# Performance work log

Hardware: AMD Instinct MI355X
Metric: run time of the kernel (lower is better)

Reference implementation:

```python
import jax, jax.numpy as jnp
import numpy as np

N_NODES = 100000
N_EDGES = 1200000
D_IN = 64
D_OUT = 64


def setup_inputs() -> dict:
    key = jax.random.key(0)
    ks = jax.random.split(key, 8)
    feat = jax.random.normal(ks[0], (N_NODES, D_IN), dtype=jnp.float32)
    src = jax.random.randint(ks[1], (N_EDGES,), 0, N_NODES, dtype=jnp.int32)
    dst = jax.random.randint(ks[2], (N_EDGES,), 0, N_NODES, dtype=jnp.int32)
    edge_weight = jax.random.uniform(ks[3], (N_EDGES, 1), dtype=jnp.float32)
    edge_mask = jax.random.uniform(ks[4], (N_EDGES, 1), dtype=jnp.float32)
    W_self = jax.random.normal(ks[5], (D_OUT, D_IN), dtype=jnp.float32) * (1.0 / np.sqrt(D_IN))
    b_self = jnp.zeros((D_OUT,), dtype=jnp.float32)
    W_neigh = jax.random.normal(ks[6], (D_OUT, D_IN), dtype=jnp.float32) * (1.0 / np.sqrt(D_IN))
    b_neigh = jnp.zeros((D_OUT,), dtype=jnp.float32)
    return {"feat": feat, "src": src, "dst": dst, "edge_weight": edge_weight,
            "edge_mask": edge_mask, "W_self": W_self, "b_self": b_self,
            "W_neigh": W_neigh, "b_neigh": b_neigh}


def reference(feat, src, dst, edge_weight, edge_mask, W_self, b_self, W_neigh, b_neigh):
    # message: gather src feats, scale by per-edge weight and mask  -> [E, D_IN]
    msg = feat[src] * edge_weight * edge_mask
    # mean scatter-reduce over incoming edges per dst node
    neigh_sum = jax.ops.segment_sum(msg, dst, num_segments=N_NODES)  # [N, D_IN]
    deg = jax.ops.segment_sum(jnp.ones((msg.shape[0],), dtype=feat.dtype), dst,
                              num_segments=N_NODES)  # [N]
    h_neigh = neigh_sum / jnp.maximum(deg, 1.0)[:, None]  # zero-degree nodes -> 0 (DGL mean semantics)
    # dual linear fuse
    rst = (feat @ W_self.T + b_self) + (h_neigh @ W_neigh.T + b_neigh)
    return rst
```

## Files before the change

### kernel.cpp

```cpp
#include <hip/hip_runtime.h>

#define NB_MAX   1568
#define CAP      1024
#define BT_EDGES 4096
#define BT_TPB   512
#define EPE      8

typedef __attribute__((ext_vector_type(4))) float floatx4;
typedef __attribute__((ext_vector_type(8))) short bf16x8;

__device__ __forceinline__ unsigned short f32_to_bf16(float f) {
  unsigned u = __float_as_uint(f);
  u = (u + 0x7fffu + ((u >> 16) & 1u)) >> 16;
  return (unsigned short)u;
}
__device__ __forceinline__ float bf16lo(unsigned u) {
  return __uint_as_float(u << 16);
}
__device__ __forceinline__ float bf16hi(unsigned u) {
  return __uint_as_float(u & 0xffff0000u);
}
__device__ __forceinline__ unsigned pack2(float a, float b) {
  return (unsigned)f32_to_bf16(a) | ((unsigned)f32_to_bf16(b) << 16);
}
__device__ __forceinline__ bf16x8 zero_bf16x8() {
  bf16x8 v;
#pragma unroll
  for (int i = 0; i < 8; ++i) v[i] = 0;
  return v;
}

__global__ __launch_bounds__(BT_TPB) void k_build(
    const float* __restrict__ feat, const int* __restrict__ src,
    const int* __restrict__ dst, const float* __restrict__ ew,
    const float* __restrict__ em, const float* __restrict__ Ws,
    const float* __restrict__ Wn, int* __restrict__ gCursor,
    uint2* __restrict__ recs, unsigned short* __restrict__ featb,
    unsigned short* __restrict__ Wb, int E, int nChunks, int nB) {
  __shared__ unsigned stageA[BT_EDGES];
  __shared__ unsigned short stageW[BT_EDGES];
  __shared__ int A[NB_MAX];
  __shared__ int B[NB_MAX];
  __shared__ int waveSums[8];

  const int t = threadIdx.x;
  const int lane = t & 63;
  const int wvid = t >> 6;
  const int e0 = blockIdx.x * BT_EDGES;
  const int eEnd = min(e0 + BT_EDGES, E);
  const int nLocal = eEnd - e0;

  for (int i = t; i < NB_MAX; i += BT_TPB) B[i] = 0;
  __syncthreads();

  int dreg[EPE];
#pragma unroll
  for (int k = 0; k < EPE; ++k) {
    int i = e0 + k * BT_TPB + t;
    dreg[k] = -1;
    if (i < eEnd) {
      int d = dst[i];
      dreg[k] = d;
      atomicAdd(&B[d >> 6], 1);
    }
  }
  __syncthreads();

  {
    const int EPT = 4;
    int b0 = t * EPT;
    int v[EPT];
    int sum = 0;
#pragma unroll
    for (int j = 0; j < EPT; ++j) {
      v[j] = (b0 + j < nB) ? B[b0 + j] : 0;
      sum += v[j];
    }
    int x = sum;
#pragma unroll
    for (int d = 1; d < 64; d <<= 1) {
      int y = __shfl_up(x, d, 64);
      if (lane >= d) x += y;
    }
    if (lane == 63) waveSums[wvid] = x;
    __syncthreads();
    int wprefix = 0;
    for (int i = 0; i < wvid; ++i) wprefix += waveSums[i];
    int run = wprefix + x - sum;
#pragma unroll
    for (int j = 0; j < EPT; ++j) {
      if (b0 + j < nB) A[b0 + j] = run;
      run += v[j];
    }
  }
  __syncthreads();

  for (int i = t; i < nB; i += BT_TPB) {
    int c = B[i];
    int l = A[i];
    int g = c ? atomicAdd(&gCursor[i], c) : 0;
    A[i] = i * CAP + g - l;
    B[i] = l;
  }
  __syncthreads();

#pragma unroll
  for (int k = 0; k < EPE; ++k) {
    int i = e0 + k * BT_TPB + t;
    if (i < eEnd) {
      int d = dreg[k];
      int r = atomicAdd(&B[d >> 6], 1);
      stageA[r] = (unsigned)src[i] | ((unsigned)(d & 63) << 17);
      float w = ew[i] * em[i];
      int wf = (int)(w * 65535.0f + 0.5f);
      stageW[r] = (unsigned short)min(wf, 65535);
    }
  }
  __syncthreads();

  for (int i = t; i < nLocal; i += BT_TPB) {
    int lo = 0, hi = nB;
    while (lo < hi) {
      int mid = (lo + hi) >> 1;
      if (B[mid] > i) hi = mid; else lo = mid + 1;
    }
    int pos = A[lo] + i;
    if (pos < (lo + 1) * CAP)
      recs[pos] = make_uint2(stageA[i], (unsigned)stageW[i]);
  }

  for (int c = blockIdx.x * BT_TPB + t; c < nChunks; c += gridDim.x * BT_TPB) {
    const float4* fp = reinterpret_cast<const float4*>(feat) + (size_t)c * 2;
    float4 a = fp[0], b = fp[1];
    uint4 o;
    o.x = pack2(a.x, a.y);
    o.y = pack2(a.z, a.w);
    o.z = pack2(b.x, b.y);
    o.w = pack2(b.z, b.w);
    reinterpret_cast<uint4*>(featb)[c] = o;
  }

  if (blockIdx.x == 0) {
    for (int i = t; i < 1024; i += BT_TPB) {
      int j = i >> 4, c4 = i & 15;
      float4 w4 = reinterpret_cast<const float4*>(Ws)[i];
      float4 n4 = reinterpret_cast<const float4*>(Wn)[i];
      *reinterpret_cast<uint2*>(&Wb[j * 128 + c4 * 4]) =
          make_uint2(pack2(w4.x, w4.y), pack2(w4.z, w4.w));
      *reinterpret_cast<uint2*>(&Wb[j * 128 + 64 + c4 * 4]) =
          make_uint2(pack2(n4.x, n4.y), pack2(n4.z, n4.w));
    }
  }
}

__global__ __launch_bounds__(256, 6) void sage_gather_gemm(
    const unsigned short* __restrict__ featb,
    const unsigned short* __restrict__ Wb, const int* __restrict__ gCursor,
    const uint2* __restrict__ recs, const float* __restrict__ bs,
    const float* __restrict__ bn, float* __restrict__ out, int N) {
  __shared__ unsigned short An[64][72];
  __shared__ uint2 recsL[CAP];
  __shared__ int cntS[64], offS[64], curS[64];

  const int t = threadIdx.x;
  const int b = blockIdx.x;
  const int n0 = b * 64;
  const int base = b * CAP;
  const int cb = min(gCursor[b], CAP);

  if (t < 64) cntS[t] = 0;
  __syncthreads();

  for (int i = t; i < cb; i += 256)
    atomicAdd(&cntS[(recs[base + i].x >> 17) & 63], 1);
  __syncthreads();

  if (t < 64) {
    int c = cntS[t];
    int x = c;
#pragma unroll
    for (int d = 1; d < 64; d <<= 1) {
      int y = __shfl_up(x, d, 64);
      if (t >= d) x += y;
    }
    offS[t] = x - c;
    curS[t] = x - c;
  }
  __syncthreads();

  for (int i = t; i < cb; i += 256) {
    uint2 rec = recs[base + i];
    int r = atomicAdd(&curS[(rec.x >> 17) & 63], 1);
    recsL[r] = rec;
  }
  __syncthreads();

  {
    int nl = t >> 2, q = t & 3;
    int deg = cntS[nl], off = offS[nl];
    float acc[16];
#pragma unroll
    for (int i = 0; i < 16; ++i) acc[i] = 0.f;
    const uint4* fb = reinterpret_cast<const uint4*>(featb);
    for (int j = 0; j < deg; ++j) {
      uint2 rec = recsL[off + j];
      int s = rec.x & 0x1FFFF;
      float w = (float)rec.y * (1.0f / 65535.0f);
      const uint4* fr = fb + (size_t)s * 8 + q * 2;
      uint4 u0 = fr[0], u1 = fr[1];
      acc[0]  += w * bf16lo(u0.x); acc[1]  += w * bf16hi(u0.x);
      acc[2]  += w * bf16lo(u0.y); acc[3]  += w * bf16hi(u0.y);
      acc[4]  += w * bf16lo(u0.z); acc[5]  += w * bf16hi(u0.z);
      acc[6]  += w * bf16lo(u0.w); acc[7]  += w * bf16hi(u0.w);
      acc[8]  += w * bf16lo(u1.x); acc[9]  += w * bf16hi(u1.x);
      acc[10] += w * bf16lo(u1.y); acc[11] += w * bf16hi(u1.y);
      acc[12] += w * bf16lo(u1.z); acc[13] += w * bf16hi(u1.z);
      acc[14] += w * bf16lo(u1.w); acc[15] += w * bf16hi(u1.w);
    }
    float inv = 1.0f / fmaxf((float)deg, 1.0f);
    uint4 o0, o1;
    o0.x = pack2(acc[0] * inv, acc[1] * inv);
    o0.y = pack2(acc[2] * inv, acc[3] * inv);
    o0.z = pack2(acc[4] * inv, acc[5] * inv);
    o0.w = pack2(acc[6] * inv, acc[7] * inv);
    o1.x = pack2(acc[8] * inv, acc[9] * inv);
    o1.y = pack2(acc[10] * inv, acc[11] * inv);
    o1.z = pack2(acc[12] * inv, acc[13] * inv);
    o1.w = pack2(acc[14] * inv, acc[15] * inv);
    *reinterpret_cast<uint4*>(&An[nl][q * 16]) = o0;
    *reinterpret_cast<uint4*>(&An[nl][q * 16 + 8]) = o1;
  }
  __syncthreads();

  const int wv = t >> 6;
  const int ln = t & 63;
  const int col = ln & 15;
  const int quad = ln >> 4;
  const int gn = n0 + wv * 16 + col;

  floatx4 acc4[4];
#pragma unroll
  for (int jt = 0; jt < 4; ++jt) {
    float bb = bs[jt * 16 + col] + bn[jt * 16 + col];
    acc4[jt] = (floatx4){bb, bb, bb, bb};
  }

#pragma unroll
  for (int kk = 0; kk < 4; ++kk) {
    bf16x8 af;
    if (kk < 2) {
      if (gn < N) {
        af = *reinterpret_cast<const bf16x8*>(featb + (size_t)gn * 64 + kk * 32 + quad * 8);
      } else {
        af = zero_bf16x8();
      }
    } else {
      af = *reinterpret_cast<const bf16x8*>(&An[wv * 16 + col][(kk - 2) * 32 + quad * 8]);
    }
#pragma unroll
    for (int jt = 0; jt < 4; ++jt) {
      bf16x8 bf = *reinterpret_cast<const bf16x8*>(
          Wb + (jt * 16 + col) * 128 + kk * 32 + quad * 8);
      acc4[jt] = __builtin_amdgcn_mfma_f32_16x16x32_bf16(af, bf, acc4[jt], 0, 0, 0);
    }
  }

#pragma unroll
  for (int jt = 0; jt < 4; ++jt) {
#pragma unroll
    for (int r = 0; r < 4; ++r) {
      int m = quad * 4 + r;
      int g = n0 + wv * 16 + m;
      if (g < N) out[(size_t)g * 64 + jt * 16 + col] = acc4[jt][r];
    }
  }
}

extern "C" void kernel_launch(void* const* d_in, const int* in_sizes, int n_in,
                              void* d_out, int out_size, void* d_ws, size_t ws_size,
                              hipStream_t stream) {
  const float* feat = (const float*)d_in[0];
  const int*   src  = (const int*)d_in[1];
  const int*   dst  = (const int*)d_in[2];
  const float* ew   = (const float*)d_in[3];
  const float* em   = (const float*)d_in[4];
  const float* Ws   = (const float*)d_in[5];
  const float* bs   = (const float*)d_in[6];
  const float* Wn   = (const float*)d_in[7];
  const float* bn   = (const float*)d_in[8];
  float* out = (float*)d_out;

  const int N = in_sizes[0] / 64;
  const int E = in_sizes[1];
  const int nB = (N + 63) / 64;

  unsigned short* featb = (unsigned short*)d_ws;
  unsigned short* Wb    = featb + (size_t)N * 64;
  uint2* recs    = (uint2*)(Wb + 64 * 128);
  int*   gCursor = (int*)(recs + (size_t)NB_MAX * CAP);

  hipMemsetAsync(gCursor, 0, NB_MAX * sizeof(int), stream);

  int nChunks = N * 8;
  int gB = (E + BT_EDGES - 1) / BT_EDGES;

  k_build<<<gB, BT_TPB, 0, stream>>>(feat, src, dst, ew, em, Ws, Wn,
                                     gCursor, recs, featb, Wb, E, nChunks, nB);
  sage_gather_gemm<<<nB, 256, 0, stream>>>(featb, Wb, gCursor, recs,
                                           bs, bn, out, N);
}
```

Baseline: 162.2 us.

## Prefetch neighbor rows two ahead and hoist edge loads before bucketing

In the gather kernel, the neighbor-feature loop now software-pipelines the irregular bf16 row loads, keeping two rows in flight so memory latency overlaps the FMAs. This raises register use, and the occupancy hint in launch_bounds is dropped to make room. In the bucketing kernel, the feat/weight bf16 conversion now runs first. The src and weight loads are pulled into the first pass over dst and held in registers, so global loads are no longer issued after the scan.

```diff
diff --git a/kernel.cpp b/kernel.cpp
--- a/kernel.cpp
+++ b/kernel.cpp
@@ -50,85 +50,6 @@
   const int eEnd = min(e0 + BT_EDGES, E);
   const int nLocal = eEnd - e0;
 
-  for (int i = t; i < NB_MAX; i += BT_TPB) B[i] = 0;
-  __syncthreads();
-
-  int dreg[EPE];
-#pragma unroll
-  for (int k = 0; k < EPE; ++k) {
-    int i = e0 + k * BT_TPB + t;
-    dreg[k] = -1;
-    if (i < eEnd) {
-      int d = dst[i];
-      dreg[k] = d;
-      atomicAdd(&B[d >> 6], 1);
-    }
-  }
-  __syncthreads();
-
-  {
-    const int EPT = 4;
-    int b0 = t * EPT;
-    int v[EPT];
-    int sum = 0;
-#pragma unroll
-    for (int j = 0; j < EPT; ++j) {
-      v[j] = (b0 + j < nB) ? B[b0 + j] : 0;
-      sum += v[j];
-    }
-    int x = sum;
-#pragma unroll
-    for (int d = 1; d < 64; d <<= 1) {
-      int y = __shfl_up(x, d, 64);
-      if (lane >= d) x += y;
-    }
-    if (lane == 63) waveSums[wvid] = x;
-    __syncthreads();
-    int wprefix = 0;
-    for (int i = 0; i < wvid; ++i) wprefix += waveSums[i];
-    int run = wprefix + x - sum;
-#pragma unroll
-    for (int j = 0; j < EPT; ++j) {
-      if (b0 + j < nB) A[b0 + j] = run;
-      run += v[j];
-    }
-  }
-  __syncthreads();
-
-  for (int i = t; i < nB; i += BT_TPB) {
-    int c = B[i];
-    int l = A[i];
-    int g = c ? atomicAdd(&gCursor[i], c) : 0;
-    A[i] = i * CAP + g - l;
-    B[i] = l;
-  }
-  __syncthreads();
-
-#pragma unroll
-  for (int k = 0; k < EPE; ++k) {
-    int i = e0 + k * BT_TPB + t;
-    if (i < eEnd) {
-      int d = dreg[k];
-      int r = atomicAdd(&B[d >> 6], 1);
-      stageA[r] = (unsigned)src[i] | ((unsigned)(d & 63) << 17);
-      float w = ew[i] * em[i];
-      int wf = (int)(w * 65535.0f + 0.5f);
-      stageW[r] = (unsigned short)min(wf, 65535);
-    }
-  }
-  __syncthreads();
-
-  for (int i = t; i < nLocal; i += BT_TPB) {
-    int lo = 0, hi = nB;
-    while (lo < hi) {
-      int mid = (lo + hi) >> 1;
-      if (B[mid] > i) hi = mid; else lo = mid + 1;
-    }
-    int pos = A[lo] + i;
-    if (pos < (lo + 1) * CAP)
-      recs[pos] = make_uint2(stageA[i], (unsigned)stageW[i]);
-  }
-
   for (int c = blockIdx.x * BT_TPB + t; c < nChunks; c += gridDim.x * BT_TPB) {
     const float4* fp = reinterpret_cast<const float4*>(feat) + (size_t)c * 2;
     float4 a = fp[0], b = fp[1];
@@ -139,7 +60,6 @@
     o.w = pack2(b.z, b.w);
     reinterpret_cast<uint4*>(featb)[c] = o;
   }
-
   if (blockIdx.x == 0) {
     for (int i = t; i < 1024; i += BT_TPB) {
       int j = i >> 4, c4 = i & 15;
@@ -151,9 +71,90 @@
           make_uint2(pack2(n4.x, n4.y), pack2(n4.z, n4.w));
     }
   }
-}
-
-__global__ __launch_bounds__(256, 6) void sage_gather_gemm(
+
+  for (int i = t; i < NB_MAX; i += BT_TPB) B[i] = 0;
+  __syncthreads();
+
+  int dreg[EPE];
+  unsigned xreg[EPE];
+  unsigned short wreg[EPE];
+#pragma unroll
+  for (int k = 0; k < EPE; ++k) {
+    int i = e0 + k * BT_TPB + t;
+    dreg[k] = -1;
+    if (i < eEnd) {
+      int d = dst[i];
+      dreg[k] = d;
+      atomicAdd(&B[d >> 6], 1);
+      xreg[k] = (unsigned)src[i] | ((unsigned)(d & 63) << 17);
+      float w = ew[i] * em[i];
+      int wf = (int)(w * 65535.0f + 0.5f);
+      wreg[k] = (unsigned short)min(wf, 65535);
+    }
+  }
+  __syncthreads();
+
+  {
+    const int EPT = 4;
+    int b0 = t * EPT;
+    int v[EPT];
+    int sum = 0;
+#pragma unroll
+    for (int j = 0; j < EPT; ++j) {
+      v[j] = (b0 + j < nB) ? B[b0 + j] : 0;
+      sum += v[j];
+    }
+    int x = sum;
+#pragma unroll
+    for (int d = 1; d < 64; d <<= 1) {
+      int y = __shfl_up(x, d, 64);
+      if (lane >= d) x += y;
+    }
+    if (lane == 63) waveSums[wvid] = x;
+    __syncthreads();
+    int wprefix = 0;
+    for (int i = 0; i < wvid; ++i) wprefix += waveSums[i];
+    int run = wprefix + x - sum;
+#pragma unroll
+    for (int j = 0; j < EPT; ++j) {
+      if (b0 + j < nB) A[b0 + j] = run;
+      run += v[j];
+    }
+  }
+  __syncthreads();
+
+  for (int i = t; i < nB; i += BT_TPB) {
+    int c = B[i];
+    int l = A[i];
+    int g = c ? atomicAdd(&gCursor[i], c) : 0;
+    A[i] = i * CAP + g - l;
+    B[i] = l;
+  }
+  __syncthreads();
+
+#pragma unroll
+  for (int k = 0; k < EPE; ++k) {
+    if (dreg[k] >= 0) {
+      int r = atomicAdd(&B[dreg[k] >> 6], 1);
+      stageA[r] = xreg[k];
+      stageW[r] = wreg[k];
+    }
+  }
+  __syncthreads();
+
+  for (int i = t; i < nLocal; i += BT_TPB) {
+    int lo = 0, hi = nB;
+    while (lo < hi) {
+      int mid = (lo + hi) >> 1;
+      if (B[mid] > i) hi = mid; else lo = mid + 1;
+    }
+    int pos = A[lo] + i;
+    if (pos < (lo + 1) * CAP)
+      recs[pos] = make_uint2(stageA[i], (unsigned)stageW[i]);
+  }
+}
+
+__global__ __launch_bounds__(256) void sage_gather_gemm(
     const unsigned short* __restrict__ featb,
     const unsigned short* __restrict__ Wb, const int* __restrict__ gCursor,
     const uint2* __restrict__ recs, const float* __restrict__ bs,
@@ -202,12 +203,31 @@
 #pragma unroll
     for (int i = 0; i < 16; ++i) acc[i] = 0.f;
     const uint4* fb = reinterpret_cast<const uint4*>(featb);
+
+    uint4 c0, c1, p0, p1;
+    float cw = 0.f, pw = 0.f;
+    if (deg > 0) {
+      uint2 r0 = recsL[off];
+      const uint4* f0 = fb + (size_t)(r0.x & 0x1FFFF) * 8 + q * 2;
+      c0 = f0[0]; c1 = f0[1];
+      cw = (float)r0.y * (1.0f / 65535.0f);
+    }
+    if (deg > 1) {
+      uint2 r1 = recsL[off + 1];
+      const uint4* f1 = fb + (size_t)(r1.x & 0x1FFFF) * 8 + q * 2;
+      p0 = f1[0]; p1 = f1[1];
+      pw = (float)r1.y * (1.0f / 65535.0f);
+    }
     for (int j = 0; j < deg; ++j) {
-      uint2 rec = recsL[off + j];
-      int s = rec.x & 0x1FFFF;
-      float w = (float)rec.y * (1.0f / 65535.0f);
-      const uint4* fr = fb + (size_t)s * 8 + q * 2;
-      uint4 u0 = fr[0], u1 = fr[1];
+      uint4 u0 = c0, u1 = c1;
+      float w = cw;
+      c0 = p0; c1 = p1; cw = pw;
+      if (j + 2 < deg) {
+        uint2 rn = recsL[off + j + 2];
+        const uint4* fn = fb + (size_t)(rn.x & 0x1FFFF) * 8 + q * 2;
+        p0 = fn[0]; p1 = fn[1];
+        pw = (float)rn.y * (1.0f / 65535.0f);
+      }
       acc[0]  += w * bf16lo(u0.x); acc[1]  += w * bf16hi(u0.x);
       acc[2]  += w * bf16lo(u0.y); acc[3]  += w * bf16hi(u0.y);
       acc[4]  += w * bf16lo(u0.z); acc[5]  += w * bf16hi(u0.z);
```

New measurement: 167.7 us. 3.4% more time.

## Gather neighbor features in FP8 with packed 9-bit edge weights and prefetch

Applied to the files above, without the earlier changes.

Adds an FP8 copy of node features that the neighbor gather reads in place of the bf16 rows, halving bytes per gathered row. Packs each edge record into one 32-bit word by quantizing the weight to 9 bits, and stages records in shared memory. Adds a two-deep software prefetch of upcoming feature rows. This trades accuracy (FP8 features, 9-bit weights) for less gather traffic and costs an extra FP8 write pass in the build kernel; the occupancy hint on launch bounds is also removed.

```diff
diff --git a/kernel.cpp b/kernel.cpp
--- a/kernel.cpp
+++ b/kernel.cpp
@@ -7,6 +7,7 @@
 #define EPE      8
 
 typedef __attribute__((ext_vector_type(4))) float floatx4;
+typedef __attribute__((ext_vector_type(2))) float floatx2;
 typedef __attribute__((ext_vector_type(8))) short bf16x8;
 
 __device__ __forceinline__ unsigned short f32_to_bf16(float f) {
@@ -14,12 +15,6 @@
   u = (u + 0x7fffu + ((u >> 16) & 1u)) >> 16;
   return (unsigned short)u;
 }
-__device__ __forceinline__ float bf16lo(unsigned u) {
-  return __uint_as_float(u << 16);
-}
-__device__ __forceinline__ float bf16hi(unsigned u) {
-  return __uint_as_float(u & 0xffff0000u);
-}
 __device__ __forceinline__ unsigned pack2(float a, float b) {
   return (unsigned)f32_to_bf16(a) | ((unsigned)f32_to_bf16(b) << 16);
 }
@@ -29,16 +24,64 @@
   for (int i = 0; i < 8; ++i) v[i] = 0;
   return v;
 }
+
+#if __has_builtin(__builtin_amdgcn_cvt_pk_fp8_f32)
+__device__ __forceinline__ unsigned pack_fp8x4(float a, float b, float c, float d) {
+  unsigned v = (unsigned)__builtin_amdgcn_cvt_pk_fp8_f32(a, b, 0, false);
+  v = (unsigned)__builtin_amdgcn_cvt_pk_fp8_f32(c, d, (int)v, true);
+  return v;
+}
+#else
+__device__ __forceinline__ unsigned sw_f32_fp8(float f) {
+  unsigned u = __float_as_uint(f);
+  unsigned s = (u >> 24) & 0x80u;
+  unsigned au = u & 0x7fffffffu;
+  if (au > 0x43E00000u) au = 0x43E00000u;
+  au += 0x7FFFFu + ((au >> 20) & 1u);
+  int e = (int)(au >> 23) - 120;
+  if (e <= 0) return s;
+  return s | ((unsigned)e << 3) | ((au >> 20) & 7u);
+}
+__device__ __forceinline__ unsigned pack_fp8x4(float a, float b, float c, float d) {
+  return sw_f32_fp8(a) | (sw_f32_fp8(b) << 8) | (sw_f32_fp8(c) << 16) |
+         (sw_f32_fp8(d) << 24);
+}
+#endif
+
+#if __has_builtin(__builtin_amdgcn_cvt_pk_f32_fp8)
+__device__ __forceinline__ void dec4(float* acc, unsigned w32, float wt) {
+  floatx2 f0 = __builtin_amdgcn_cvt_pk_f32_fp8((int)w32, false);
+  floatx2 f1 = __builtin_amdgcn_cvt_pk_f32_fp8((int)w32, true);
+  acc[0] += wt * f0.x; acc[1] += wt * f0.y;
+  acc[2] += wt * f1.x; acc[3] += wt * f1.y;
+}
+#else
+__device__ __forceinline__ float sw_fp8_f32(unsigned b) {
+  unsigned s = (b & 0x80u) << 24;
+  unsigned e = (b >> 3) & 0xFu;
+  unsigned m = b & 7u;
+  float fn = __uint_as_float(s | ((e + 120u) << 23) | (m << 20));
+  float fd = (float)(int)m * 0.001953125f;
+  fd = (b & 0x80u) ? -fd : fd;
+  return e ? fn : fd;
+}
+__device__ __forceinline__ void dec4(float* acc, unsigned w32, float wt) {
+  acc[0] += wt * sw_fp8_f32(w32 & 0xFF);
+  acc[1] += wt * sw_fp8_f32((w32 >> 8) & 0xFF);
+  acc[2] += wt * sw_fp8_f32((w32 >> 16) & 0xFF);
+  acc[3] += wt * sw_fp8_f32(w32 >> 24);
+}
+#endif
 
 __global__ __launch_bounds__(BT_TPB) void k_build(
     const float* __restrict__ feat, const int* __restrict__ src,
     const int* __restrict__ dst, const float* __restrict__ ew,
     const float* __restrict__ em, const float* __restrict__ Ws,
     const float* __restrict__ Wn, int* __restrict__ gCursor,
-    uint2* __restrict__ recs, unsigned short* __restrict__ featb,
-    unsigned short* __restrict__ Wb, int E, int nChunks, int nB) {
-  __shared__ unsigned stageA[BT_EDGES];
-  __shared__ unsigned short stageW[BT_EDGES];
+    unsigned* __restrict__ recs, unsigned short* __restrict__ featb,
+    unsigned char* __restrict__ featq, unsigned short* __restrict__ Wb,
+    int E, int nChunks, int nB) {
+  __shared__ unsigned stage[BT_EDGES];
   __shared__ int A[NB_MAX];
   __shared__ int B[NB_MAX];
   __shared__ int waveSums[8];
@@ -110,10 +153,11 @@
     if (i < eEnd) {
       int d = dreg[k];
       int r = atomicAdd(&B[d >> 6], 1);
-      stageA[r] = (unsigned)src[i] | ((unsigned)(d & 63) << 17);
       float w = ew[i] * em[i];
-      int wf = (int)(w * 65535.0f + 0.5f);
-      stageW[r] = (unsigned short)min(wf, 65535);
+      int wq = (int)(w * 511.0f + 0.5f);
+      if (wq > 511) wq = 511;
+      stage[r] = (unsigned)src[i] | ((unsigned)(d & 63) << 17) |
+                 ((unsigned)wq << 23);
     }
   }
   __syncthreads();
@@ -126,7 +170,7 @@
     }
     int pos = A[lo] + i;
     if (pos < (lo + 1) * CAP)
-      recs[pos] = make_uint2(stageA[i], (unsigned)stageW[i]);
+      recs[pos] = stage[i];
   }
 
   for (int c = blockIdx.x * BT_TPB + t; c < nChunks; c += gridDim.x * BT_TPB) {
@@ -138,6 +182,10 @@
     o.z = pack2(b.x, b.y);
     o.w = pack2(b.z, b.w);
     reinterpret_cast<uint4*>(featb)[c] = o;
+    uint2 q8;
+    q8.x = pack_fp8x4(a.x, a.y, a.z, a.w);
+    q8.y = pack_fp8x4(b.x, b.y, b.z, b.w);
+    reinterpret_cast<uint2*>(featq)[c] = q8;
   }
 
   if (blockIdx.x == 0) {
@@ -153,13 +201,15 @@
   }
 }
 
-__global__ __launch_bounds__(256, 6) void sage_gather_gemm(
+__global__ __launch_bounds__(256) void sage_gather_gemm(
     const unsigned short* __restrict__ featb,
+    const unsigned char* __restrict__ featq,
     const unsigned short* __restrict__ Wb, const int* __restrict__ gCursor,
-    const uint2* __restrict__ recs, const float* __restrict__ bs,
+    const unsigned* __restrict__ recs, const float* __restrict__ bs,
     const float* __restrict__ bn, float* __restrict__ out, int N) {
   __shared__ unsigned short An[64][72];
-  __shared__ uint2 recsL[CAP];
+  __shared__ unsigned rawL[CAP];
+  __shared__ unsigned srtL[CAP];
   __shared__ int cntS[64], offS[64], curS[64];
 
   const int t = threadIdx.x;
@@ -168,11 +218,12 @@
   const int base = b * CAP;
   const int cb = min(gCursor[b], CAP);
 
+  for (int i = t; i < cb; i += 256) rawL[i] = recs[base + i];
   if (t < 64) cntS[t] = 0;
   __syncthreads();
 
   for (int i = t; i < cb; i += 256)
-    atomicAdd(&cntS[(recs[base + i].x >> 17) & 63], 1);
+    atomicAdd(&cntS[(rawL[i] >> 17) & 63], 1);
   __syncthreads();
 
   if (t < 64) {
@@ -189,9 +240,9 @@
   __syncthreads();
 
   for (int i = t; i < cb; i += 256) {
-    uint2 rec = recs[base + i];
-    int r = atomicAdd(&curS[(rec.x >> 17) & 63], 1);
-    recsL[r] = rec;
+    unsigned r = rawL[i];
+    int p = atomicAdd(&curS[(r >> 17) & 63], 1);
+    srtL[p] = r;
   }
   __syncthreads();
 
@@ -201,21 +252,33 @@
     float acc[16];
 #pragma unroll
     for (int i = 0; i < 16; ++i) acc[i] = 0.f;
-    const uint4* fb = reinterpret_cast<const uint4*>(featb);
+    const uint4* fq = reinterpret_cast<const uint4*>(featq);
+
+    uint4 uC, uN;
+    float wC = 0.f, wN = 0.f;
+    if (deg > 0) {
+      unsigned r0 = srtL[off];
+      uC = fq[(size_t)(r0 & 0x1FFFF) * 4 + q];
+      wC = (float)(r0 >> 23) * (1.0f / 511.0f);
+    }
+    if (deg > 1) {
+      unsigned r1 = srtL[off + 1];
+      uN = fq[(size_t)(r1 & 0x1FFFF) * 4 + q];
+      wN = (float)(r1 >> 23) * (1.0f / 511.0f);
+    }
     for (int j = 0; j < deg; ++j) {
-      uint2 rec = recsL[off + j];
-      int s = rec.x & 0x1FFFF;
-      float w = (float)rec.y * (1.0f / 65535.0f);
-      const uint4* fr = fb + (size_t)s * 8 + q * 2;
-      uint4 u0 = fr[0], u1 = fr[1];
-      acc[0]  += w * bf16lo(u0.x); acc[1]  += w * bf16hi(u0.x);
-      acc[2]  += w * bf16lo(u0.y); acc[3]  += w * bf16hi(u0.y);
-      acc[4]  += w * bf16lo(u0.z); acc[5]  += w * bf16hi(u0.z);
-      acc[6]  += w * bf16lo(u0.w); acc[7]  += w * bf16hi(u0.w);
-      acc[8]  += w * bf16lo(u1.x); acc[9]  += w * bf16hi(u1.x);
-      acc[10] += w * bf16lo(u1.y); acc[11] += w * bf16hi(u1.y);
-      acc[12] += w * bf16lo(u1.z); acc[13] += w * bf16hi(u1.z);
-      acc[14] += w * bf16lo(u1.w); acc[15] += w * bf16hi(u1.w);
+      uint4 u = uC;
+      float w = wC;
+      uC = uN; wC = wN;
+      if (j + 2 < deg) {
+        unsigned rn = srtL[off + j + 2];
+        uN = fq[(size_t)(rn & 0x1FFFF) * 4 + q];
+        wN = (float)(rn >> 23) * (1.0f / 511.0f);
+      }
+      dec4(acc + 0, u.x, w);
+      dec4(acc + 4, u.y, w);
+      dec4(acc + 8, u.z, w);
+      dec4(acc + 12, u.w, w);
     }
     float inv = 1.0f / fmaxf((float)deg, 1.0f);
     uint4 o0, o1;
@@ -295,9 +358,10 @@
   const int nB = (N + 63) / 64;
 
   unsigned short* featb = (unsigned short*)d_ws;
-  unsigned short* Wb    = featb + (size_t)N * 64;
-  uint2* recs    = (uint2*)(Wb + 64 * 128);
-  int*   gCursor = (int*)(recs + (size_t)NB_MAX * CAP);
+  unsigned char*  featq = (unsigned char*)(featb + (size_t)N * 64);
+  unsigned short* Wb    = (unsigned short*)(featq + (size_t)N * 64);
+  unsigned* recs   = (unsigned*)(Wb + 64 * 128);
+  int*      gCursor = (int*)(recs + (size_t)NB_MAX * CAP);
 
   hipMemsetAsync(gCursor, 0, NB_MAX * sizeof(int), stream);
 
@@ -305,7 +369,8 @@
   int gB = (E + BT_EDGES - 1) / BT_EDGES;
 
   k_build<<<gB, BT_TPB, 0, stream>>>(feat, src, dst, ew, em, Ws, Wn,
-                                     gCursor, recs, featb, Wb, E, nChunks, nB);
-  sage_gather_gemm<<<nB, 256, 0, stream>>>(featb, Wb, gCursor, recs,
+                                     gCursor, recs, featb, featq, Wb,
+                                     E, nChunks, nB);
+  sage_gather_gemm<<<nB, 256, 0, stream>>>(featb, featq, Wb, gCursor, recs,
                                            bs, bn, out, N);
 }
```

Result: no change. 163.8 us (+1.0%).
